# Kernel optimization log

Hardware: AMD Instinct MI355X
Metric: run time of the kernel (lower is better)

The kernel has to match this reference:

```python
import jax, jax.numpy as jnp
import numpy as np

N0, N1, N2, N3 = 400000, 100000, 20000, 4096
IN_F, HID_F, OUT_F = 256, 256, 128
E0, E1, E2 = 1500000, 200000, 40960


def setup_inputs() -> dict:
    key = jax.random.key(0)
    ks = jax.random.split(key, 16)
    inp = {}
    inp['feat'] = jax.random.normal(ks[0], (N0, IN_F), dtype=jnp.float32)
    inp['e0_src'] = jax.random.randint(ks[1], (E0,), 0, N0)
    inp['e0_dst'] = jax.random.randint(ks[2], (E0,), 0, N1)
    inp['e1_src'] = jax.random.randint(ks[3], (E1,), 0, N1)
    inp['e1_dst'] = jax.random.randint(ks[4], (E1,), 0, N2)
    inp['e2_src'] = jax.random.randint(ks[5], (E2,), 0, N2)
    inp['e2_dst'] = jax.random.randint(ks[6], (E2,), 0, N3)
    # SAGEConv params: fc_self and fc_neigh weights (in,out) + shared bias
    def lin(k, fi, fo):
        s = 1.0 / np.sqrt(fi)
        return jax.random.uniform(k, (fi, fo), jnp.float32, -s, s)
    inp['w_self0'] = lin(ks[7], IN_F, HID_F)
    inp['w_neigh0'] = lin(ks[8], IN_F, HID_F)
    inp['b0'] = jnp.zeros((HID_F,), jnp.float32)
    inp['w_self1'] = lin(ks[9], HID_F, HID_F)
    inp['w_neigh1'] = lin(ks[10], HID_F, HID_F)
    inp['b1'] = jnp.zeros((HID_F,), jnp.float32)
    inp['w_self2'] = lin(ks[11], HID_F, OUT_F)
    inp['w_neigh2'] = lin(ks[12], HID_F, OUT_F)
    inp['b2'] = jnp.zeros((OUT_F,), jnp.float32)
    return inp


def _sage_conv(h, src, dst, n_dst, w_self, w_neigh, b, act):
    # mean aggregation of src-node features onto dst nodes (irregular gather + segment reduce)
    msgs = h[src]                                                  # [E, F]
    s = jax.ops.segment_sum(msgs, dst, num_segments=n_dst)        # [n_dst, F]
    cnt = jax.ops.segment_sum(jnp.ones((src.shape[0], 1), h.dtype), dst, num_segments=n_dst)
    h_neigh = s / jnp.maximum(cnt, 1.0)
    out = h[:n_dst] @ w_self + h_neigh @ w_neigh + b
    return jax.nn.relu(out) if act else out


def reference(feat, e0_src, e0_dst, e1_src, e1_dst, e2_src, e2_dst,
              w_self0, w_neigh0, b0, w_self1, w_neigh1, b1, w_self2, w_neigh2, b2):
    # dropout is identity (eval mode)
    h = _sage_conv(feat, e0_src, e0_dst, N1, w_self0, w_neigh0, b0, act=True)
    h = _sage_conv(h, e1_src, e1_dst, N2, w_self1, w_neigh1, b1, act=True)
    h = _sage_conv(h, e2_src, e2_dst, N3, w_self2, w_neigh2, b2, act=False)
    return h
```

## Files before the change

kernel.cpp:

```cpp
#include <hip/hip_runtime.h>
#include <hip/hip_bf16.h>


static constexpr int kN1 = 100000, kN2 = 20000, kN3 = 4096;
static constexpr int kE0 = 1500000, kE1 = 200000, kE2 = 40960;

using bf8v  = __attribute__((ext_vector_type(8))) short;
using f32x4 = __attribute__((ext_vector_type(4))) float;

__device__ __forceinline__ unsigned short f2bu(float f) {
    __hip_bfloat16 h = __float2bfloat16(f);
    return *reinterpret_cast<unsigned short*>(&h);
}
__device__ __forceinline__ float bu2f_lo(unsigned u) {
    unsigned b = u << 16; return *reinterpret_cast<float*>(&b);
}
__device__ __forceinline__ float bu2f_hi(unsigned u) {
    unsigned b = u & 0xffff0000u; return *reinterpret_cast<float*>(&b);
}

static constexpr int CB  = 50000;
static constexpr int C0B = (kE0 + 255) / 256;
static constexpr int C1B = (kE1 + 255) / 256;
static constexpr int C2B = (kE2 + 255) / 256;
static constexpr int PW0B = 512, PW1B = 512, PW2B = 256;
static constexpr int M4_0 = kN1 / 4, M4_1 = kN2 / 4, M4_2 = kN3 / 4;
static constexpr int B0 = (M4_0 + 255) / 256;
static constexpr int B1 = (M4_1 + 255) / 256;
static constexpr int B2 = (M4_2 + 255) / 256;
static constexpr int BSCAN = B0 + B1 + B2;
static constexpr int ZN4 = 496384 / 16;
static constexpr int ZB  = (ZN4 + 255) / 256;
static constexpr int ET = kE0 + kE1 + kE2;
static constexpr int FB = (ET / 8 + 255) / 256;

__global__ __launch_bounds__(256) void k_zero(int4* __restrict__ p)
{
    int i = blockIdx.x * 256 + threadIdx.x;
    if (i < ZN4) p[i] = make_int4(0, 0, 0, 0);
}

template <bool BIG>
__global__ __launch_bounds__(256) void k_phase0(
    const float4* __restrict__ feat4, uint4* __restrict__ featbf,
    const int* __restrict__ e0d, const int* __restrict__ e1d,
    const int* __restrict__ e2d,
    int* __restrict__ cnt0, int* __restrict__ cnt1, int* __restrict__ cnt2,
    int* __restrict__ er0, int* __restrict__ er1, int* __restrict__ er2,
    const float* __restrict__ ws0, const float* __restrict__ wn0,
    const float* __restrict__ ws1, const float* __restrict__ wn1,
    const float* __restrict__ ws2, const float* __restrict__ wn2,
    unsigned short* __restrict__ wt0, unsigned short* __restrict__ wt1,
    unsigned short* __restrict__ wt2)
{
    int b = blockIdx.x;
    const int tid = threadIdx.x;
    if (BIG) {
        if (b < CB) {
            int i = b * 256 + tid;
            float4 a = feat4[2 * i], c = feat4[2 * i + 1];
            uint4 o;
            o.x = (unsigned)f2bu(a.x) | ((unsigned)f2bu(a.y) << 16);
            o.y = (unsigned)f2bu(a.z) | ((unsigned)f2bu(a.w) << 16);
            o.z = (unsigned)f2bu(c.x) | ((unsigned)f2bu(c.y) << 16);
            o.w = (unsigned)f2bu(c.z) | ((unsigned)f2bu(c.w) << 16);
            featbf[i] = o;
            return;
        }
        b -= CB;
    }
    if (b < C0B) {
        int e = b * 256 + tid;
        if (e < kE0) er0[e] = atomicAdd(cnt0 + e0d[e], 1);
        return;
    }
    b -= C0B;
    if (b < C1B) {
        int e = b * 256 + tid;
        if (e < kE1) er1[e] = atomicAdd(cnt1 + e1d[e], 1);
        return;
    }
    b -= C1B;
    if (b < C2B) {
        int e = b * 256 + tid;
        if (e < kE2) er2[e] = atomicAdd(cnt2 + e2d[e], 1);
        return;
    }
    b -= C2B;
    if (b < PW0B) {
        int idx = b * 256 + tid;
        int n = idx >> 9, k = idx & 511;
        wt0[idx] = f2bu(k < 256 ? ws0[k * 256 + n] : wn0[(k - 256) * 256 + n]);
        return;
    }
    b -= PW0B;
    if (b < PW1B) {
        int idx = b * 256 + tid;
        int n = idx >> 9, k = idx & 511;
        wt1[idx] = f2bu(k < 256 ? ws1[k * 256 + n] : wn1[(k - 256) * 256 + n]);
        return;
    }
    b -= PW1B;
    {
        int idx = b * 256 + tid;
        int n = idx >> 9, k = idx & 511;
        wt2[idx] = f2bu(k < 256 ? ws2[k * 128 + n] : wn2[(k - 256) * 128 + n]);
    }
}

__global__ __launch_bounds__(256) void k_bsum_all(
    const int* __restrict__ cnt0, const int* __restrict__ cnt1,
    const int* __restrict__ cnt2, int* __restrict__ bsum)
{
    const int* cnt; int lb, M4, bo;
    int b = blockIdx.x;
    if (b < B0)            { cnt = cnt0; lb = b;            M4 = M4_0; bo = 0; }
    else if (b < B0 + B1)  { cnt = cnt1; lb = b - B0;       M4 = M4_1; bo = B0; }
    else                   { cnt = cnt2; lb = b - B0 - B1;  M4 = M4_2; bo = B0 + B1; }
    __shared__ int wsum[4];
    int idx = lb * 256 + threadIdx.x;
    int ts = 0;
    if (idx < M4) {
        int4 v = reinterpret_cast<const int4*>(cnt)[idx];
        ts = v.x + v.y + v.z + v.w;
    }
#pragma unroll
    for (int off = 32; off > 0; off >>= 1) ts += __shfl_down(ts, off, 64);
    if ((threadIdx.x & 63) == 0) wsum[threadIdx.x >> 6] = ts;
    __syncthreads();
    if (threadIdx.x == 0)
        bsum[bo + lb] = wsum[0] + wsum[1] + wsum[2] + wsum[3];
}

__global__ __launch_bounds__(256) void k_bapply_all(
    const int* __restrict__ cnt0, const int* __restrict__ cnt1,
    const int* __restrict__ cnt2, const int* __restrict__ bsum,
    int* __restrict__ rp0, int* __restrict__ rp1, int* __restrict__ rp2)
{
    const int* cnt; int* rp; int lb, M4, lo;
    int b = blockIdx.x;
    if (b < B0)            { cnt = cnt0; rp = rp0; lb = b;           M4 = M4_0; lo = 0; }
    else if (b < B0 + B1)  { cnt = cnt1; rp = rp1; lb = b - B0;      M4 = M4_1; lo = B0; }
    else                   { cnt = cnt2; rp = rp2; lb = b - B0 - B1; M4 = M4_2; lo = B0 + B1; }
    __shared__ int sscan[BSCAN];
    __shared__ int wsum[4];
    __shared__ int wexcl[4];
    __shared__ int blockbase;
    const int tid = threadIdx.x;
    const int lane = tid & 63;
    const int wid = tid >> 6;
    if (tid < BSCAN) sscan[tid] = bsum[tid];
    __syncthreads();
    if (tid == 0) {
        int s = 0;
        for (int i = lo; i < lo + lb; ++i) s += sscan[i];
        blockbase = s;
    }
    int idx = lb * 256 + tid;
    int4 v = make_int4(0, 0, 0, 0);
    if (idx < M4) v = reinterpret_cast<const int4*>(cnt)[idx];
    int ts = v.x + v.y + v.z + v.w;
    int incl = ts;
#pragma unroll
    for (int off = 1; off < 64; off <<= 1) {
        int t = __shfl_up(incl, off, 64);
        if (lane >= off) incl += t;
    }
    if (lane == 63) wsum[wid] = incl;
    __syncthreads();
    if (tid < 4) {
        int e = 0;
        for (int i = 0; i < tid; ++i) e += wsum[i];
        wexcl[tid] = e;
    }
    __syncthreads();
    if (idx < M4) {
        int base = blockbase + wexcl[wid] + (incl - ts);
        int4 o;
        o.x = base;
        o.y = base + v.x;
        o.z = base + v.x + v.y;
        o.w = base + v.x + v.y + v.z;
        reinterpret_cast<int4*>(rp)[idx] = o;
    }
}

__global__ __launch_bounds__(256) void k_fill_all(
    const int* __restrict__ e0s, const int* __restrict__ e0d,
    const int* __restrict__ e1s, const int* __restrict__ e1d,
    const int* __restrict__ e2s, const int* __restrict__ e2d,
    const int* __restrict__ er0, const int* __restrict__ er1,
    const int* __restrict__ er2,
    const int* __restrict__ rp0, const int* __restrict__ rp1,
    const int* __restrict__ rp2,
    int* __restrict__ csr0, int* __restrict__ csr1, int* __restrict__ csr2)
{
    const int t = blockIdx.x * 256 + threadIdx.x;
    const int T = FB * 256;
    int ss[8], dd[8], rr[8], pos[8];
    const int* rpp[8];
    int* cp[8];
    bool ok[8];
#pragma unroll
    for (int i = 0; i < 8; ++i) {
        int e = t + i * T;
        ok[i] = e < ET;
        ss[i] = 0; dd[i] = 0; rr[i] = 0; rpp[i] = rp0; cp[i] = csr0;
        if (ok[i]) {
            if (e < kE0) {
                ss[i] = e0s[e]; dd[i] = e0d[e]; rr[i] = er0[e];
            } else if (e < kE0 + kE1) {
                int le = e - kE0;
                ss[i] = e1s[le]; dd[i] = e1d[le]; rr[i] = er1[le];
                rpp[i] = rp1; cp[i] = csr1;
            } else {
                int le = e - kE0 - kE1;
                ss[i] = e2s[le]; dd[i] = e2d[le]; rr[i] = er2[le];
                rpp[i] = rp2; cp[i] = csr2;
            }
        }
    }
#pragma unroll
    for (int i = 0; i < 8; ++i)
        if (ok[i]) pos[i] = rpp[i][dd[i]];
#pragma unroll
    for (int i = 0; i < 8; ++i)
        if (ok[i]) cp[i][pos[i] + rr[i]] = ss[i];
}

__global__ __launch_bounds__(256) void k_gather_agg_b(
    const unsigned short* __restrict__ h, const int* __restrict__ csr,
    const int* __restrict__ rp_start, const int* __restrict__ cnt,
    unsigned short* __restrict__ agg, int M)
{
    int d = blockIdx.x * 4 + (threadIdx.x >> 6);
    if (d >= M) return;
    const int lane = threadIdx.x & 63;
    const int half = lane >> 5;
    const int l32 = lane & 31;
    int c = cnt[d], start = rp_start[d], end = start + c;
    float a[8] = {0.f, 0.f, 0.f, 0.f, 0.f, 0.f, 0.f, 0.f};
    for (int chunk = start; chunk < end; chunk += 64) {
        int n = end - chunk; if (n > 64) n = 64;
        int mysrc = (lane < n) ? csr[chunk + lane] : 0;
#pragma unroll 4
        for (int e = 0; e < n; e += 2) {
            int ie = e + half;
            int s = __shfl(mysrc, ie, 64);
            if (ie < n) {
                uint4 v = *reinterpret_cast<const uint4*>(
                    h + (size_t)s * 256 + l32 * 8);
                a[0] += bu2f_lo(v.x); a[1] += bu2f_hi(v.x);
                a[2] += bu2f_lo(v.y); a[3] += bu2f_hi(v.y);
                a[4] += bu2f_lo(v.z); a[5] += bu2f_hi(v.z);
                a[6] += bu2f_lo(v.w); a[7] += bu2f_hi(v.w);
            }
        }
    }
#pragma unroll
    for (int j = 0; j < 8; ++j) a[j] += __shfl(a[j], lane ^ 32, 64);
    if (half == 0) {
        float inv = 1.0f / (float)(c > 1 ? c : 1);
        uint4 o;
        o.x = (unsigned)f2bu(a[0] * inv) | ((unsigned)f2bu(a[1] * inv) << 16);
        o.y = (unsigned)f2bu(a[2] * inv) | ((unsigned)f2bu(a[3] * inv) << 16);
        o.z = (unsigned)f2bu(a[4] * inv) | ((unsigned)f2bu(a[5] * inv) << 16);
        o.w = (unsigned)f2bu(a[6] * inv) | ((unsigned)f2bu(a[7] * inv) << 16);
        *reinterpret_cast<uint4*>(agg + (size_t)d * 256 + l32 * 8) = o;
    }
}

__global__ __launch_bounds__(256) void k_gather_agg_f(
    const float* __restrict__ h, const int* __restrict__ csr,
    const int* __restrict__ rp_start, const int* __restrict__ cnt,
    unsigned short* __restrict__ agg, int M)
{
    int d = blockIdx.x * 4 + (threadIdx.x >> 6);
    if (d >= M) return;
    int lane = threadIdx.x & 63;
    int c = cnt[d], start = rp_start[d], end = start + c;
    float a0 = 0.f, a1 = 0.f, a2 = 0.f, a3 = 0.f;
    for (int chunk = start; chunk < end; chunk += 64) {
        int n = end - chunk; if (n > 64) n = 64;
        int mysrc = (lane < n) ? csr[chunk + lane] : 0;
#pragma unroll 4
        for (int e = 0; e < n; ++e) {
            int s = __shfl(mysrc, e, 64);
            float4 v = reinterpret_cast<const float4*>(h + (size_t)s * 256)[lane];
            a0 += v.x; a1 += v.y; a2 += v.z; a3 += v.w;
        }
    }
    float inv = 1.0f / (float)(c > 1 ? c : 1);
    ushort4 o;
    o.x = f2bu(a0 * inv); o.y = f2bu(a1 * inv);
    o.z = f2bu(a2 * inv); o.w = f2bu(a3 * inv);
    *reinterpret_cast<ushort4*>(agg + (size_t)d * 256 + lane * 4) = o;
}

template <int ACT, bool A0F32, bool OUTF32>
__global__ __launch_bounds__(256) void k_mfma_gemm(
    const void* __restrict__ A0v, const unsigned short* __restrict__ A1,
    const unsigned short* __restrict__ WT, const float* __restrict__ bias,
    void* __restrict__ outv, int M, int N)
{
    __shared__ unsigned short sA[128 * 72];
    __shared__ unsigned short sB[128 * 72];
    const int tid = threadIdx.x;
    const int lane = tid & 63;
    const int w = tid >> 6;
    const int wr = w >> 1, wc = w & 1;
    const int row0 = blockIdx.x * 128;
    const int col0 = blockIdx.y * 128;

    f32x4 acc[4][4] = {};

    for (int p = 0; p < 8; ++p) {
        const int kc0 = p * 64;
        if (kc0 < 256) {
            if constexpr (A0F32) {
                const float* src = (const float*)A0v;
#pragma unroll
                for (int ps = 0; ps < 8; ++ps) {
                    int flat = (ps * 256 + tid) * 4;
                    int r = flat >> 6, cc = flat & 63;
                    int row = row0 + r; row = row < M ? row : M - 1;
                    float4 v = *reinterpret_cast<const float4*>(
                        src + (size_t)row * 256 + kc0 + cc);
                    ushort4 b4;
                    b4.x = f2bu(v.x); b4.y = f2bu(v.y);
                    b4.z = f2bu(v.z); b4.w = f2bu(v.w);
                    *reinterpret_cast<ushort4*>(&sA[r * 72 + cc]) = b4;
                }
            } else {
                const unsigned short* src = (const unsigned short*)A0v;
#pragma unroll
                for (int ps = 0; ps < 4; ++ps) {
                    int f8 = ps * 256 + tid;
                    int r = f8 >> 3, c8 = f8 & 7;
                    int row = row0 + r; row = row < M ? row : M - 1;
                    uint4 v = *reinterpret_cast<const uint4*>(
                        src + (size_t)row * 256 + kc0 + c8 * 8);
                    *reinterpret_cast<uint4*>(&sA[r * 72 + c8 * 8]) = v;
                }
            }
        } else {
#pragma unroll
            for (int ps = 0; ps < 4; ++ps) {
                int f8 = ps * 256 + tid;
                int r = f8 >> 3, c8 = f8 & 7;
                int row = row0 + r; row = row < M ? row : M - 1;
                uint4 v = *reinterpret_cast<const uint4*>(
                    A1 + (size_t)row * 256 + (kc0 - 256) + c8 * 8);
                *reinterpret_cast<uint4*>(&sA[r * 72 + c8 * 8]) = v;
            }
        }
#pragma unroll
        for (int ps = 0; ps < 4; ++ps) {
            int f8 = ps * 256 + tid;
            int r = f8 >> 3, c8 = f8 & 7;
            uint4 v = *reinterpret_cast<const uint4*>(
                WT + (size_t)(col0 + r) * 512 + kc0 + c8 * 8);
            *reinterpret_cast<uint4*>(&sB[r * 72 + c8 * 8]) = v;
        }
        __syncthreads();
#pragma unroll
        for (int ks = 0; ks < 64; ks += 32) {
            const int lr = lane & 15;
            const int kk = ks + (lane >> 4) * 8;
            bf8v af[4], bfr[4];
#pragma unroll
            for (int m = 0; m < 4; ++m)
                af[m] = *reinterpret_cast<const bf8v*>(
                    &sA[(wr * 64 + m * 16 + lr) * 72 + kk]);
#pragma unroll
            for (int n = 0; n < 4; ++n)
                bfr[n] = *reinterpret_cast<const bf8v*>(
                    &sB[(wc * 64 + n * 16 + lr) * 72 + kk]);
#pragma unroll
            for (int m = 0; m < 4; ++m)
#pragma unroll
                for (int n = 0; n < 4; ++n)
                    acc[m][n] = __builtin_amdgcn_mfma_f32_16x16x32_bf16(
                        af[m], bfr[n], acc[m][n], 0, 0, 0);
        }
        __syncthreads();
    }

    const int lc = lane & 15;
    const int lr4 = (lane >> 4) * 4;
#pragma unroll
    for (int n = 0; n < 4; ++n) {
        int col = col0 + wc * 64 + n * 16 + lc;
        float bb = bias[col];
#pragma unroll
        for (int m = 0; m < 4; ++m) {
#pragma unroll
            for (int j = 0; j < 4; ++j) {
                int row = row0 + wr * 64 + m * 16 + lr4 + j;
                if (row < M) {
                    float v = acc[m][n][j] + bb;
                    if (ACT) v = fmaxf(v, 0.f);
                    if constexpr (OUTF32)
                        ((float*)outv)[(size_t)row * N + col] = v;
                    else
                        ((unsigned short*)outv)[(size_t)row * N + col] = f2bu(v);
                }
            }
        }
    }
}

extern "C" void kernel_launch(void* const* d_in, const int* in_sizes, int n_in,
                              void* d_out, int out_size, void* d_ws, size_t ws_size,
                              hipStream_t stream) {
    const float* feat = (const float*)d_in[0];
    const int* e0s = (const int*)d_in[1];
    const int* e0d = (const int*)d_in[2];
    const int* e1s = (const int*)d_in[3];
    const int* e1d = (const int*)d_in[4];
    const int* e2s = (const int*)d_in[5];
    const int* e2d = (const int*)d_in[6];
    const float* ws0 = (const float*)d_in[7];
    const float* wn0 = (const float*)d_in[8];
    const float* b0 = (const float*)d_in[9];
    const float* ws1 = (const float*)d_in[10];
    const float* wn1 = (const float*)d_in[11];
    const float* b1 = (const float*)d_in[12];
    const float* ws2 = (const float*)d_in[13];
    const float* wn2 = (const float*)d_in[14];
    const float* b2 = (const float*)d_in[15];
    float* out = (float*)d_out;

    char* base = (char*)d_ws;
    const bool big = ws_size >= 345000000ull;
    unsigned short* featbf = nullptr;
    size_t off = 0;
    if (big) { featbf = (unsigned short*)base; off += 204800000ull; }
    unsigned short* aggb = (unsigned short*)(base + off); off += 51200000ull;
    unsigned short* h1b  = (unsigned short*)(base + off); off += 51200000ull;
    unsigned short* h2b  = (unsigned short*)(base + off); off += 10240000ull;
    unsigned short* wt0  = (unsigned short*)(base + off); off += 262144ull;
    unsigned short* wt1  = (unsigned short*)(base + off); off += 262144ull;
    unsigned short* wt2  = (unsigned short*)(base + off); off += 131072ull;
    int* csr0 = (int*)(base + off); off += 6000000ull;
    int* csr1 = (int*)(base + off); off += 800000ull;
    int* csr2 = (int*)(base + off); off += 163840ull;
    int* cnt0 = (int*)(base + off); off += 400000ull;
    int* cnt1 = (int*)(base + off); off += 80000ull;
    int* cnt2 = (int*)(base + off); off += 16384ull;
    int* rp0  = (int*)(base + off); off += 400000ull;
    int* rp1  = (int*)(base + off); off += 80000ull;
    int* rp2  = (int*)(base + off); off += 16384ull;
    int* bsum = (int*)(base + off); off += 512ull;
    int* er0  = (int*)(base + off); off += 6000000ull;
    int* er1  = (int*)(base + off); off += 800000ull;
    int* er2  = (int*)(base + off); off += 163840ull;

    k_zero<<<ZB, 256, 0, stream>>>((int4*)cnt0);

    if (big)
        k_phase0<true><<<CB + C0B + C1B + C2B + PW0B + PW1B + PW2B, 256, 0, stream>>>(
            (const float4*)feat, (uint4*)featbf, e0d, e1d, e2d,
            cnt0, cnt1, cnt2, er0, er1, er2,
            ws0, wn0, ws1, wn1, ws2, wn2, wt0, wt1, wt2);
    else
        k_phase0<false><<<C0B + C1B + C2B + PW0B + PW1B + PW2B, 256, 0, stream>>>(
            nullptr, nullptr, e0d, e1d, e2d,
            cnt0, cnt1, cnt2, er0, er1, er2,
            ws0, wn0, ws1, wn1, ws2, wn2, wt0, wt1, wt2);

    k_bsum_all<<<BSCAN, 256, 0, stream>>>(cnt0, cnt1, cnt2, bsum);
    k_bapply_all<<<BSCAN, 256, 0, stream>>>(
        cnt0, cnt1, cnt2, bsum, rp0, rp1, rp2);
    k_fill_all<<<FB, 256, 0, stream>>>(
        e0s, e0d, e1s, e1d, e2s, e2d,
        er0, er1, er2, rp0, rp1, rp2, csr0, csr1, csr2);

    if (big) {
        k_gather_agg_b<<<(kN1 + 3) / 4, 256, 0, stream>>>(
            featbf, csr0, rp0, cnt0, aggb, kN1);
        k_mfma_gemm<1, false, false><<<dim3(782, 2), 256, 0, stream>>>(
            featbf, aggb, wt0, b0, h1b, kN1, 256);
    } else {
        k_gather_agg_f<<<(kN1 + 3) / 4, 256, 0, stream>>>(
            feat, csr0, rp0, cnt0, aggb, kN1);
        k_mfma_gemm<1, true, false><<<dim3(782, 2), 256, 0, stream>>>(
            feat, aggb, wt0, b0, h1b, kN1, 256);
    }

    k_gather_agg_b<<<(kN2 + 3) / 4, 256, 0, stream>>>(
        h1b, csr1, rp1, cnt1, aggb, kN2);
    k_mfma_gemm<1, false, false><<<dim3(157, 2), 256, 0, stream>>>(
        h1b, aggb, wt1, b1, h2b, kN2, 256);

    k_gather_agg_b<<<(kN3 + 3) / 4, 256, 0, stream>>>(
        h2b, csr2, rp2, cnt2, aggb, kN3);
    k_mfma_gemm<0, false, true><<<dim3(32, 1), 256, 0, stream>>>(
        h2b, aggb, wt2, b2, out, kN3, 128);
}
```

Before: 472.5 us.

## Merge scan kernels, add nontemporal stores, raise gather unroll

```diff
diff --git a/kernel.cpp b/kernel.cpp
--- a/kernel.cpp
+++ b/kernel.cpp
@@ -7,6 +7,7 @@
 
 using bf8v  = __attribute__((ext_vector_type(8))) short;
 using f32x4 = __attribute__((ext_vector_type(4))) float;
+using u32x4 = __attribute__((ext_vector_type(4))) unsigned int;
 
 __device__ __forceinline__ unsigned short f2bu(float f) {
     __hip_bfloat16 h = __float2bfloat16(f);
@@ -108,57 +109,35 @@
     }
 }
 
-__global__ __launch_bounds__(256) void k_bsum_all(
+__global__ __launch_bounds__(256) void k_scan_apply(
     const int* __restrict__ cnt0, const int* __restrict__ cnt1,
-    const int* __restrict__ cnt2, int* __restrict__ bsum)
-{
-    const int* cnt; int lb, M4, bo;
+    const int* __restrict__ cnt2,
+    int* __restrict__ rp0, int* __restrict__ rp1, int* __restrict__ rp2)
+{
+    const int* cnt; int* rp; int lb, M4;
     int b = blockIdx.x;
-    if (b < B0)            { cnt = cnt0; lb = b;            M4 = M4_0; bo = 0; }
-    else if (b < B0 + B1)  { cnt = cnt1; lb = b - B0;       M4 = M4_1; bo = B0; }
-    else                   { cnt = cnt2; lb = b - B0 - B1;  M4 = M4_2; bo = B0 + B1; }
-    __shared__ int wsum[4];
-    int idx = lb * 256 + threadIdx.x;
-    int ts = 0;
-    if (idx < M4) {
-        int4 v = reinterpret_cast<const int4*>(cnt)[idx];
-        ts = v.x + v.y + v.z + v.w;
-    }
-#pragma unroll
-    for (int off = 32; off > 0; off >>= 1) ts += __shfl_down(ts, off, 64);
-    if ((threadIdx.x & 63) == 0) wsum[threadIdx.x >> 6] = ts;
-    __syncthreads();
-    if (threadIdx.x == 0)
-        bsum[bo + lb] = wsum[0] + wsum[1] + wsum[2] + wsum[3];
-}
-
-__global__ __launch_bounds__(256) void k_bapply_all(
-    const int* __restrict__ cnt0, const int* __restrict__ cnt1,
-    const int* __restrict__ cnt2, const int* __restrict__ bsum,
-    int* __restrict__ rp0, int* __restrict__ rp1, int* __restrict__ rp2)
-{
-    const int* cnt; int* rp; int lb, M4, lo;
-    int b = blockIdx.x;
-    if (b < B0)            { cnt = cnt0; rp = rp0; lb = b;           M4 = M4_0; lo = 0; }
-    else if (b < B0 + B1)  { cnt = cnt1; rp = rp1; lb = b - B0;      M4 = M4_1; lo = B0; }
-    else                   { cnt = cnt2; rp = rp2; lb = b - B0 - B1; M4 = M4_2; lo = B0 + B1; }
-    __shared__ int sscan[BSCAN];
+    if (b < B0)            { cnt = cnt0; rp = rp0; lb = b;           M4 = M4_0; }
+    else if (b < B0 + B1)  { cnt = cnt1; rp = rp1; lb = b - B0;      M4 = M4_1; }
+    else                   { cnt = cnt2; rp = rp2; lb = b - B0 - B1; M4 = M4_2; }
+    const int tid = threadIdx.x;
+    const int lane = tid & 63;
+    const int wid = tid >> 6;
+    __shared__ int wpre[4];
     __shared__ int wsum[4];
     __shared__ int wexcl[4];
     __shared__ int blockbase;
-    const int tid = threadIdx.x;
-    const int lane = tid & 63;
-    const int wid = tid >> 6;
-    if (tid < BSCAN) sscan[tid] = bsum[tid];
-    __syncthreads();
-    if (tid == 0) {
-        int s = 0;
-        for (int i = lo; i < lo + lb; ++i) s += sscan[i];
-        blockbase = s;
-    }
+    const int4* c4 = reinterpret_cast<const int4*>(cnt);
+    int pre = 0;
+    for (int i = tid; i < lb * 256; i += 256) {
+        int4 v = c4[i];
+        pre += v.x + v.y + v.z + v.w;
+    }
+#pragma unroll
+    for (int off = 32; off > 0; off >>= 1) pre += __shfl_down(pre, off, 64);
+    if (lane == 0) wpre[wid] = pre;
     int idx = lb * 256 + tid;
     int4 v = make_int4(0, 0, 0, 0);
-    if (idx < M4) v = reinterpret_cast<const int4*>(cnt)[idx];
+    if (idx < M4) v = c4[idx];
     int ts = v.x + v.y + v.z + v.w;
     int incl = ts;
 #pragma unroll
@@ -168,6 +147,7 @@
     }
     if (lane == 63) wsum[wid] = incl;
     __syncthreads();
+    if (tid == 0) blockbase = wpre[0] + wpre[1] + wpre[2] + wpre[3];
     if (tid < 4) {
         int e = 0;
         for (int i = 0; i < tid; ++i) e += wsum[i];
@@ -225,7 +205,7 @@
         if (ok[i]) pos[i] = rpp[i][dd[i]];
 #pragma unroll
     for (int i = 0; i < 8; ++i)
-        if (ok[i]) cp[i][pos[i] + rr[i]] = ss[i];
+        if (ok[i]) __builtin_nontemporal_store(ss[i], &cp[i][pos[i] + rr[i]]);
 }
 
 __global__ __launch_bounds__(256) void k_gather_agg_b(
@@ -243,7 +223,7 @@
     for (int chunk = start; chunk < end; chunk += 64) {
         int n = end - chunk; if (n > 64) n = 64;
         int mysrc = (lane < n) ? csr[chunk + lane] : 0;
-#pragma unroll 4
+#pragma unroll 8
         for (int e = 0; e < n; e += 2) {
             int ie = e + half;
             int s = __shfl(mysrc, ie, 64);
@@ -261,12 +241,13 @@
     for (int j = 0; j < 8; ++j) a[j] += __shfl(a[j], lane ^ 32, 64);
     if (half == 0) {
         float inv = 1.0f / (float)(c > 1 ? c : 1);
-        uint4 o;
-        o.x = (unsigned)f2bu(a[0] * inv) | ((unsigned)f2bu(a[1] * inv) << 16);
-        o.y = (unsigned)f2bu(a[2] * inv) | ((unsigned)f2bu(a[3] * inv) << 16);
-        o.z = (unsigned)f2bu(a[4] * inv) | ((unsigned)f2bu(a[5] * inv) << 16);
-        o.w = (unsigned)f2bu(a[6] * inv) | ((unsigned)f2bu(a[7] * inv) << 16);
-        *reinterpret_cast<uint4*>(agg + (size_t)d * 256 + l32 * 8) = o;
+        u32x4 o;
+        o[0] = (unsigned)f2bu(a[0] * inv) | ((unsigned)f2bu(a[1] * inv) << 16);
+        o[1] = (unsigned)f2bu(a[2] * inv) | ((unsigned)f2bu(a[3] * inv) << 16);
+        o[2] = (unsigned)f2bu(a[4] * inv) | ((unsigned)f2bu(a[5] * inv) << 16);
+        o[3] = (unsigned)f2bu(a[6] * inv) | ((unsigned)f2bu(a[7] * inv) << 16);
+        __builtin_nontemporal_store(
+            o, reinterpret_cast<u32x4*>(agg + (size_t)d * 256 + l32 * 8));
     }
 }
 
@@ -451,7 +432,6 @@
     int* rp0  = (int*)(base + off); off += 400000ull;
     int* rp1  = (int*)(base + off); off += 80000ull;
     int* rp2  = (int*)(base + off); off += 16384ull;
-    int* bsum = (int*)(base + off); off += 512ull;
     int* er0  = (int*)(base + off); off += 6000000ull;
     int* er1  = (int*)(base + off); off += 800000ull;
     int* er2  = (int*)(base + off); off += 163840ull;
@@ -469,9 +449,8 @@
             cnt0, cnt1, cnt2, er0, er1, er2,
             ws0, wn0, ws1, wn1, ws2, wn2, wt0, wt1, wt2);
 
-    k_bsum_all<<<BSCAN, 256, 0, stream>>>(cnt0, cnt1, cnt2, bsum);
-    k_bapply_all<<<BSCAN, 256, 0, stream>>>(
-        cnt0, cnt1, cnt2, bsum, rp0, rp1, rp2);
+    k_scan_apply<<<BSCAN, 256, 0, stream>>>(
+        cnt0, cnt1, cnt2, rp0, rp1, rp2);
     k_fill_all<<<FB, 256, 0, stream>>>(
         e0s, e0d, e1s, e1d, e2s, e2d,
         er0, er1, er2, rp0, rp1, rp2, csr0, csr1, csr2);
```

Result: slower. 514.1 us (+8.8%).
